# Kernel tuning notes

Measured on AMD Instinct MI355X. Metric: run time of the kernel, lower is better.

Reference implementation:

```python
import jax, jax.numpy as jnp
import numpy as np

# ---- constants from the source module ----
NB = [[0,1,2,3],[0,1,4],[0,2,5],[0,3,6],[1,4,7],[2,5,8],[3,6,9],[4,7,10],[5,8,11],[6,9],[7,10],[8,11],[12,13,14,15],[12,13,16],[12,14,17],[12,15],[13,16,18],[14,17,19],[16,18,20],[17,19,21],[18,20,22],[19,21,23],[20,22],[21,23]]
PARENT = np.array([0,0,0,0,1,2,3,4,5,6,7,8,9,9,9,12,13,14,16,17,18,19,20,21])  # root parent sentinel handled separately
KJ, NV, PREG = 24, 6890, 200
LEN = np.array([len(n) for n in NB])
NBR_IDX = np.zeros((KJ,4), np.int32)
NBR_VALID = np.zeros((KJ,4), np.float32)
for k, n in enumerate(NB):
    NBR_IDX[k,:len(n)] = n; NBR_VALID[k,:len(n)] = 1.0
BETA_POS = np.zeros((KJ,17), np.float32); BETA_POS[np.arange(KJ), 4*LEN] = 1.0
SLICE_MASK = np.zeros((23,17), np.float32)
for j in range(23):
    SLICE_MASK[j,:4*LEN[j]+1] = 1.0  # self.K[j] has 4*len(NB[j])+1 rows
NBR_IDX = jnp.asarray(NBR_IDX); NBR_VALID = jnp.asarray(NBR_VALID)
BETA_POS = jnp.asarray(BETA_POS); SLICE_MASK = jnpp = jnp.asarray(SLICE_MASK)


def setup_inputs() -> dict:
    key = jax.random.key(0)
    ks = jax.random.split(key, 9)
    V = jax.random.normal(ks[0], (PREG, NV, 3), jnp.float32)
    T = jax.random.normal(ks[1], (PREG, NV, 3), jnp.float32)
    J = jax.random.normal(ks[2], (PREG, KJ, 3), jnp.float32)
    theta = 0.3 * jax.random.normal(ks[3], (PREG, 72), jnp.float32)
    W_prime = jax.random.uniform(ks[4], (NV, KJ), jnp.float32)
    W_i = jax.random.uniform(ks[5], (NV, KJ), jnp.float32)
    W_i = W_i / W_i.sum(axis=1, keepdims=True)
    A = jax.random.uniform(ks[6], (23, NV), jnp.float32)
    K_mats = 0.01 * jax.random.normal(ks[7], (23, 17, 3 * NV), jnp.float32)
    K_mats = K_mats * SLICE_MASK[:, :, None]  # zero rows beyond the ragged per-joint size
    beta_2 = jnp.ones((1,), jnp.float32)
    return {"V": V, "T": T, "J": J, "theta": theta, "W_prime": W_prime, "W_i": W_i, "A": A, "K_mats": K_mats, "beta_2": beta_2, "epoch": 1}


def _rodrigues(pose):  # pose: (K,3)
    angle = jnp.maximum(jnp.linalg.norm(pose, axis=1, keepdims=True), 1e-8)
    axis = pose / angle
    x, y, z = axis[:, 0], axis[:, 1], axis[:, 2]
    zero = jnp.zeros_like(x)
    skew = jnp.stack([zero, -z, y, z, zero, -x, -y, x, zero], axis=1).reshape(-1, 3, 3)
    outer = axis[:, :, None] * axis[:, None, :]
    c = jnp.cos(angle)[:, :, None]
    s = jnp.sin(angle)[:, :, None]
    eye = jnp.eye(3, dtype=pose.dtype)[None]
    return c * eye + (1.0 - c) * outer + s * skew


def _compute_G(pose72, Jp):  # pose72: (72,), Jp: (K,3) -> (K,4,4)
    R = _rodrigues(pose72.reshape(KJ, 3))
    t = Jp - jnp.concatenate([jnp.zeros((1, 3), Jp.dtype), Jp[PARENT[1:]]], axis=0)
    G_local = jnp.zeros((KJ, 4, 4), Jp.dtype)
    G_local = G_local.at[:, :3, :3].set(R).at[:, :3, 3].set(t).at[:, 3, 3].set(1.0)
    Gs = [G_local[0]]
    for i in range(1, KJ):  # fixed 24-joint kinematic tree
        Gs.append(Gs[PARENT[i]] @ G_local[i])
    G = jnp.stack(Gs, axis=0)
    off = jnp.einsum('kij,kj->ki', G[:, :3, :3], Jp)  # homogeneous w=0 -> rotation only
    return G.at[:, :3, 3].add(-off)


def _axis2quat(p):  # (M,3) -> (M,4)
    angle = jnp.sqrt(jnp.maximum(jnp.sum(p ** 2, axis=1), 1e-16))
    n = p / angle[:, None]
    s = jnp.sin(angle / 2)
    return jnp.stack([n[:, 0] * s, n[:, 1] * s, n[:, 2] * s, jnp.cos(angle / 2) - 1.0], axis=1)


def reference(V, T, J, theta, W_prime, W_i, A, K_mats, beta_2, epoch):
    P = V.shape[0]
    b2 = beta_2[0]
    # normalized skinning weights
    W_relu = jax.nn.relu(W_prime)
    W_change = W_relu / (W_relu.sum(axis=1, keepdims=True) + 1e-8)
    # per-pose global joint transforms
    G_prime = jax.vmap(_compute_G)(theta, J)  # (P,K,4,4)
    # quaternion features and blend-shape correction
    q = _axis2quat(theta.reshape(P * KJ, 3)).reshape(P, KJ, 4)
    qg = q[:, NBR_IDX, :] * NBR_VALID[None, :, :, None]       # (P,K,4,4) neighbor gather
    q17 = jnp.concatenate([qg.reshape(P, KJ, 16), jnp.zeros((P, KJ, 1), q.dtype)], axis=-1)
    q17 = q17 + BETA_POS[None] * b2                            # beta_2 at column 4*len
    qm = q17[:, 1:, :] * SLICE_MASK[None]                      # ragged slice q_ne[:, j+1, :lenK]
    contrib = jnp.einsum('pjl,jlm->pjm', qm, K_mats).reshape(P, 23, NV, 3)
    T_p = jnp.einsum('pjnc,jn->pnc', contrib, jax.nn.relu(A)) + T
    # linear blend skinning
    T_h = jnp.concatenate([T_p, jnp.ones((P, NV, 1), T_p.dtype)], axis=-1)
    transformed = jnp.einsum('pkij,pnj->pnki', G_prime[:, :, :3, :], T_h)  # (P,N,K,3)
    verts = jnp.einsum('nk,pnkc->pnc', W_change, transformed)
    # energies
    e = float(epoch)
    g_wi = 0.1 * np.exp(-0.1 * e)
    g_w = 0.002 * np.exp(-0.008 * e)
    g_a = 0.001 * np.exp(-0.008 * e)
    g_k = 0.1 * np.exp(-0.008 * e)
    E_D = jnp.sum((V - verts) ** 2)
    E_Wi = jnp.sum((W_change - W_i) ** 2)
    E_W = jnp.sum(jnp.abs(W_change))
    E_A = jnp.sum(jnp.abs(A))
    E_K = jnp.sum(jnp.sqrt(jnp.sum(K_mats ** 2, axis=(1, 2))))
    E = E_D + g_wi * E_Wi + g_w * E_W + g_a * E_A + g_k * E_K
    return (E, verts)
```

## Files before the change

kernel.cpp:

```cpp
#include <hip/hip_runtime.h>
#include <math.h>

#define KJ 24
#define NV 6890
#define PREG 200
#define M_TOT (NV*3)
#define KDIM 391
#define KPAD 416
#define TP_STRIDE 20672
#define NMT64 323
#define NSTAGE (NMT64*13)

#define EDP_OFF 0
#define EKP_OFF 5400
#define WIP_OFF 101984
#define EWP_OFF 102016
#define EAP_OFF 102048
#define RED_OFF 102080
#define G_OFF   102112
#define TP_OFF  159712
#define QBH_OFF_U 10903488
#define QBL_OFF_U 11009984
#define BTH_OFF_U 11116480
#define BTL_OFF_U 19716032
#define TP2_OFF 14157792

typedef __attribute__((ext_vector_type(8))) short short8;
typedef __attribute__((ext_vector_type(4))) float f32x4;
typedef __attribute__((ext_vector_type(4))) unsigned int u32x4;

__constant__ int c_PARENT[24] = {0,0,0,0,1,2,3,4,5,6,7,8,9,9,9,12,13,14,16,17,18,19,20,21};
__constant__ int c_DEPTH[24]  = {0,1,1,1,2,2,2,3,3,3,4,4,4,4,4,5,5,5,6,6,7,7,8,8};
__constant__ int c_LEN[24]    = {4,3,3,3,3,3,3,3,3,2,2,2,4,3,3,2,3,3,3,3,3,3,2,2};
__constant__ int c_NBR[24][4] = {
  {0,1,2,3},{0,1,4,0},{0,2,5,0},{0,3,6,0},{1,4,7,0},{2,5,8,0},{3,6,9,0},{4,7,10,0},
  {5,8,11,0},{6,9,0,0},{7,10,0,0},{8,11,0,0},{12,13,14,15},{12,13,16,0},{12,14,17,0},
  {12,15,0,0},{13,16,18,0},{14,17,19,0},{16,18,20,0},{17,19,21,0},{18,20,22,0},
  {19,21,23,0},{20,22,0,0},{21,23,0,0}};

__device__ __forceinline__ float waveReduce(float v) {
  #pragma unroll
  for (int off = 32; off > 0; off >>= 1) v += __shfl_down(v, off, 64);
  return v;
}
__device__ __forceinline__ unsigned short f2bf(float x) {
  union { float f; unsigned u; } v; v.f = x;
  unsigned r = v.u + 0x7FFFu + ((v.u >> 16) & 1u);
  return (unsigned short)(r >> 16);
}
__device__ __forceinline__ float bf2f(unsigned short h) {
  union { unsigned u; float f; } v; v.u = ((unsigned)h) << 16; return v.f;
}

__global__ __launch_bounds__(256) void kPre(const float* __restrict__ J,
                                            const float* __restrict__ theta,
                                            const float* __restrict__ beta2,
                                            const float* __restrict__ Wp,
                                            const float* __restrict__ Wi,
                                            const float* __restrict__ A,
                                            const float* __restrict__ K,
                                            float* __restrict__ ws) {
  unsigned short* qbh = (unsigned short*)ws + QBH_OFF_U;
  unsigned short* qbl = (unsigned short*)ws + QBL_OFF_U;
  int b = blockIdx.x;
  if (b < 50) {
    __shared__ float Gl[4][24][12];
    __shared__ float Gg[4][24][12];
    __shared__ float q[4][24][4];
    int w = threadIdx.x >> 6, t = threadIdx.x & 63;
    int p = b*4 + w;
    if (t < 24) {
      float x = theta[p*72 + 3*t + 0];
      float y = theta[p*72 + 3*t + 1];
      float z = theta[p*72 + 3*t + 2];
      float n2 = x*x + y*y + z*z;
      float ang = fmaxf(sqrtf(n2), 1e-8f);
      float ia = 1.f/ang;
      float ax = x*ia, ay = y*ia, az = z*ia;
      float c = cosf(ang), s = sinf(ang), C = 1.f - c;
      float jx = J[p*72+3*t], jy = J[p*72+3*t+1], jz = J[p*72+3*t+2];
      float tx = jx, ty = jy, tz = jz;
      if (t > 0) {
        int par = c_PARENT[t];
        tx -= J[p*72+3*par]; ty -= J[p*72+3*par+1]; tz -= J[p*72+3*par+2];
      }
      Gl[w][t][0]=c+C*ax*ax;   Gl[w][t][1]=C*ax*ay-s*az; Gl[w][t][2]=C*ax*az+s*ay; Gl[w][t][3]=tx;
      Gl[w][t][4]=C*ax*ay+s*az;Gl[w][t][5]=c+C*ay*ay;    Gl[w][t][6]=C*ay*az-s*ax; Gl[w][t][7]=ty;
      Gl[w][t][8]=C*ax*az-s*ay;Gl[w][t][9]=C*ay*az+s*ax; Gl[w][t][10]=c+C*az*az;   Gl[w][t][11]=tz;
      float ang2 = sqrtf(fmaxf(n2, 1e-16f));
      float inv2 = 1.f/ang2;
      float s2 = sinf(0.5f*ang2);
      q[w][t][0] = x*inv2*s2; q[w][t][1] = y*inv2*s2; q[w][t][2] = z*inv2*s2;
      q[w][t][3] = cosf(0.5f*ang2) - 1.f;
    }
    __syncthreads();
    for (int lev = 0; lev <= 8; lev++) {
      if (t < 24 && c_DEPTH[t] == lev) {
        if (lev == 0) {
          for (int i2 = 0; i2 < 12; i2++) Gg[w][0][i2] = Gl[w][0][i2];
        } else {
          int par = c_PARENT[t];
          for (int r = 0; r < 3; r++) {
            float g0 = Gg[w][par][r*4+0], g1 = Gg[w][par][r*4+1];
            float g2 = Gg[w][par][r*4+2], g3 = Gg[w][par][r*4+3];
            for (int c2 = 0; c2 < 4; c2++) {
              float v = g0*Gl[w][t][0+c2] + g1*Gl[w][t][4+c2] + g2*Gl[w][t][8+c2];
              if (c2 == 3) v += g3;
              Gg[w][t][r*4+c2] = v;
            }
          }
        }
      }
      __syncthreads();
    }
    if (t < 24) {
      float jx = J[p*72+3*t], jy = J[p*72+3*t+1], jz = J[p*72+3*t+2];
      float* gp = ws + G_OFF + p*288 + t*12;
      #pragma unroll
      for (int r = 0; r < 3; r++) {
        float off = Gg[w][t][r*4+0]*jx + Gg[w][t][r*4+1]*jy + Gg[w][t][r*4+2]*jz;
        Gg[w][t][r*4+3] -= off;
      }
      #pragma unroll
      for (int i2 = 0; i2 < 12; i2++) gp[i2] = Gg[w][t][i2];
    }
    __syncthreads();
    float b2 = beta2[0];
    for (int e = t; e < KDIM; e += 64) {
      int j = e / 17, l = e - 17*j;
      int k = j + 1;
      float val = 0.f;
      if (l < 4*c_LEN[j] + 1) {
        if (l < 16) {
          int sidx = l >> 2, cc = l & 3;
          if (sidx < c_LEN[k]) val = q[w][c_NBR[k][sidx]][cc];
        }
        if (l == 4*c_LEN[k]) val += b2;
      }
      unsigned short hi = f2bf(val);
      unsigned short lo = f2bf(val - bf2f(hi));
      qbh[p*KPAD + e] = hi;
      qbl[p*KPAD + e] = lo;
    }
    for (int e = KDIM + t; e < KPAD; e += 64) {
      qbh[p*KPAD + e] = 0; qbl[p*KPAD + e] = 0;
    }
  } else if (b < 77) {
    int d = b - 50;
    int t = threadIdx.x;
    int n = d*256 + t;
    float ewi = 0.f, ew = 0.f, ea = 0.f;
    if (n < NV) {
      float wv[24]; float sum = 0.f;
      const float4* wp4 = (const float4*)(Wp + n*24);
      #pragma unroll
      for (int i = 0; i < 6; i++) {
        float4 v4 = wp4[i];
        wv[4*i+0] = fmaxf(v4.x, 0.f); wv[4*i+1] = fmaxf(v4.y, 0.f);
        wv[4*i+2] = fmaxf(v4.z, 0.f); wv[4*i+3] = fmaxf(v4.w, 0.f);
        sum += wv[4*i+0]+wv[4*i+1]+wv[4*i+2]+wv[4*i+3];
      }
      float inv = 1.f/(sum + 1e-8f);
      #pragma unroll
      for (int k = 0; k < 24; k++) {
        float wc = wv[k]*inv;
        ew += fabsf(wc);
        float dd = wc - Wi[n*24+k];
        ewi += dd*dd;
      }
    }
    for (int i = d*256 + t; i < 23*NV; i += 27*256) ea += fabsf(A[i]);
    for (int i = d*256 + t; i < 56*KPAD; i += 27*256) {
      qbh[200*KPAD + i] = 0; qbl[200*KPAD + i] = 0;
    }
    __shared__ float red[3][4];
    int lane = t & 63, wv2 = t >> 6;
    ewi = waveReduce(ewi); ew = waveReduce(ew); ea = waveReduce(ea);
    if (lane == 0) { red[0][wv2] = ewi; red[1][wv2] = ew; red[2][wv2] = ea; }
    __syncthreads();
    if (t == 0) {
      ws[WIP_OFF + d] = red[0][0]+red[0][1]+red[0][2]+red[0][3];
      ws[EWP_OFF + d] = red[1][0]+red[1][1]+red[1][2]+red[1][3];
      ws[EAP_OFF + d] = red[2][0]+red[2][1]+red[2][2]+red[2][3];
    }
  } else {
    int flat = b - 77;
    int bx = flat % NMT64, by = flat / NMT64;
    int m0 = bx*64, kg0 = by*32;
    __shared__ unsigned short Sh[32*66];
    __shared__ unsigned short Sl[32*66];
    __shared__ float ek[23];
    int t = threadIdx.x;
    if (t < 23) ek[t] = 0.f;
    __syncthreads();
    int krow = t >> 3, mseg = (t & 7) * 8;
    int kg = kg0 + krow;
    int mm = m0 + mseg;
    float kv[8], wv[8]; float sq = 0.f;
    #pragma unroll
    for (int i = 0; i < 8; i++) { kv[i] = 0.f; wv[i] = 0.f; }
    if (kg < KDIM) {
      const float* kr = K + (size_t)kg*M_TOT + mm;
      if (mm + 7 < M_TOT) {
        float4 a4 = *(const float4*)kr; float4 b4 = *(const float4*)(kr+4);
        kv[0]=a4.x; kv[1]=a4.y; kv[2]=a4.z; kv[3]=a4.w;
        kv[4]=b4.x; kv[5]=b4.y; kv[6]=b4.z; kv[7]=b4.w;
      } else {
        #pragma unroll
        for (int i = 0; i < 8; i++) if (mm+i < M_TOT) kv[i] = kr[i];
      }
      int j = kg / 17;
      int nb = mm / 3;
      float av[4];
      #pragma unroll
      for (int i = 0; i < 4; i++)
        av[i] = (nb + i < NV) ? fmaxf(A[j*NV + nb + i], 0.f) : 0.f;
      #pragma unroll
      for (int i = 0; i < 8; i++) {
        float a = (mm+i < M_TOT) ? av[(mm+i)/3 - nb] : 0.f;
        wv[i] = kv[i]*a;
        sq = fmaf(kv[i], kv[i], sq);
      }
    }
    #pragma unroll
    for (int c = 0; c < 4; c++) {
      unsigned short h0 = f2bf(wv[2*c]),  h1 = f2bf(wv[2*c+1]);
      unsigned short l0 = f2bf(wv[2*c]   - bf2f(h0));
      unsigned short l1 = f2bf(wv[2*c+1] - bf2f(h1));
      *(unsigned*)&Sh[krow*66 + mseg + 2*c] = (unsigned)h0 | ((unsigned)h1 << 16);
      *(unsigned*)&Sl[krow*66 + mseg + 2*c] = (unsigned)l0 | ((unsigned)l1 << 16);
    }
    sq += __shfl_xor(sq, 1, 64);
    sq += __shfl_xor(sq, 2, 64);
    sq += __shfl_xor(sq, 4, 64);
    if ((t & 7) == 0 && kg < KDIM) atomicAdd(&ek[kg/17], sq);
    __syncthreads();
    int mrow = t >> 2, kq = t & 3;
    unsigned dh[4], dl[4];
    #pragma unroll
    for (int c2 = 0; c2 < 4; c2++) {
      unsigned short s0 = Sh[(kq*8 + 2*c2    )*66 + mrow];
      unsigned short s1 = Sh[(kq*8 + 2*c2 + 1)*66 + mrow];
      dh[c2] = (unsigned)s0 | ((unsigned)s1 << 16);
      unsigned short u0 = Sl[(kq*8 + 2*c2    )*66 + mrow];
      unsigned short u1 = Sl[(kq*8 + 2*c2 + 1)*66 + mrow];
      dl[c2] = (unsigned)u0 | ((unsigned)u1 << 16);
    }
    unsigned short* BtH = (unsigned short*)ws + BTH_OFF_U;
    unsigned short* BtL = (unsigned short*)ws + BTL_OFF_U;
    size_t o = (size_t)(m0 + mrow)*KPAD + kg0 + kq*8;
    *(u32x4*)(BtH + o) = (u32x4){dh[0], dh[1], dh[2], dh[3]};
    *(u32x4*)(BtL + o) = (u32x4){dl[0], dl[1], dl[2], dl[3]};
    if (t < 23) ws[EKP_OFF + t*NSTAGE + flat] = ek[t];
  }
}

template<int KS0, int NKS>
__device__ __forceinline__ void kb_body(const unsigned short* __restrict__ qbh,
                                        const unsigned short* __restrict__ qbl,
                                        const unsigned short* __restrict__ BtH,
                                        const unsigned short* __restrict__ BtL,
                                        short (*__restrict__ SBh)[64*32],
                                        short (*__restrict__ SBl)[64*32],
                                        float* __restrict__ TPd, int m0) {
  const int tid = threadIdx.x;
  const int w = tid >> 6, lane = tid & 63;
  const int r = lane & 15, qd = lane >> 4;

  f32x4 acc[4][4];
  #pragma unroll
  for (int h = 0; h < 4; h++)
    #pragma unroll
    for (int f = 0; f < 4; f++) acc[h][f] = (f32x4){0.f,0.f,0.f,0.f};

  int aofs[4];
  #pragma unroll
  for (int h = 0; h < 4; h++) aofs[h] = (w*64 + h*16 + r)*KPAD + KS0*32 + qd*8;

  const int srow = tid >> 2, sseg = tid & 3;
  const size_t gB = (size_t)(m0 + srow)*KPAD + KS0*32 + sseg*8;
  const int swr = ((srow >> 4)*64 + sseg*16 + (srow & 15)) * 8;

  short8 ah[2][4], al[2][4];
  short8 bsh[2], bsl[2];

  bsh[0] = *(const short8*)(BtH + gB);
  bsl[0] = *(const short8*)(BtL + gB);
  #pragma unroll
  for (int h = 0; h < 4; h++) {
    ah[0][h] = *(const short8*)(qbh + aofs[h]);
    al[0][h] = *(const short8*)(qbl + aofs[h]);
  }
  *(short8*)&SBh[0][swr] = bsh[0];
  *(short8*)&SBl[0][swr] = bsl[0];
  bsh[1] = *(const short8*)(BtH + gB + 32);
  bsl[1] = *(const short8*)(BtL + gB + 32);
  #pragma unroll
  for (int h = 0; h < 4; h++) {
    ah[1][h] = *(const short8*)(qbh + aofs[h] + 32);
    al[1][h] = *(const short8*)(qbl + aofs[h] + 32);
  }
  __syncthreads();

  #pragma unroll
  for (int ks = 0; ks < NKS; ks++) {
    const int cur = ks & 1, nxt = cur ^ 1;
    short8 bfh[4], bfl[4];
    #pragma unroll
    for (int f = 0; f < 4; f++) {
      bfh[f] = *(const short8*)&SBh[cur][(f*64 + lane)*8];
      bfl[f] = *(const short8*)&SBl[cur][(f*64 + lane)*8];
    }
    #pragma unroll
    for (int f = 0; f < 4; f++)
      #pragma unroll
      for (int h = 0; h < 4; h++) {
        acc[h][f] = __builtin_amdgcn_mfma_f32_16x16x32_bf16(ah[cur][h], bfh[f], acc[h][f], 0, 0, 0);
        acc[h][f] = __builtin_amdgcn_mfma_f32_16x16x32_bf16(ah[cur][h], bfl[f], acc[h][f], 0, 0, 0);
        acc[h][f] = __builtin_amdgcn_mfma_f32_16x16x32_bf16(al[cur][h], bfh[f], acc[h][f], 0, 0, 0);
      }
    if (ks + 1 < NKS) {
      *(short8*)&SBh[nxt][swr] = bsh[nxt];
      *(short8*)&SBl[nxt][swr] = bsl[nxt];
    }
    if (ks + 2 < NKS) {
      const int o = (ks + 2) * 32;
      bsh[cur] = *(const short8*)(BtH + gB + o);
      bsl[cur] = *(const short8*)(BtL + gB + o);
      #pragma unroll
      for (int h = 0; h < 4; h++) {
        ah[cur][h] = *(const short8*)(qbh + aofs[h] + o);
        al[cur][h] = *(const short8*)(qbl + aofs[h] + o);
      }
    }
    __syncthreads();
  }
  #pragma unroll
  for (int h = 0; h < 4; h++)
    #pragma unroll
    for (int f = 0; f < 4; f++)
      #pragma unroll
      for (int g = 0; g < 4; g++) {
        int p = w*64 + h*16 + qd*4 + g;
        if (p < PREG)
          TPd[(size_t)p*TP_STRIDE + m0 + f*16 + r] = acc[h][f][g];
      }
}

__global__ __launch_bounds__(256) void kB(float* __restrict__ ws) {
  __shared__ short SBh[2][64*32];
  __shared__ short SBl[2][64*32];
  const unsigned short* qbh = (const unsigned short*)ws + QBH_OFF_U;
  const unsigned short* qbl = (const unsigned short*)ws + QBL_OFF_U;
  const unsigned short* BtH = (const unsigned short*)ws + BTH_OFF_U;
  const unsigned short* BtL = (const unsigned short*)ws + BTL_OFF_U;
  const int m0 = blockIdx.x * 64;
  if (blockIdx.y == 0)
    kb_body<0, 7>(qbh, qbl, BtH, BtL, SBh, SBl, ws + TP_OFF, m0);
  else
    kb_body<7, 6>(qbh, qbl, BtH, BtL, SBh, SBl, ws + TP2_OFF, m0);
}

__global__ __launch_bounds__(256) void kC(const float* __restrict__ V,
                                          const float* __restrict__ T,
                                          const float* __restrict__ Wp,
                                          const float* __restrict__ ws,
                                          float* __restrict__ out) {
  int p0 = blockIdx.y * 8;
  int n = blockIdx.x*256 + threadIdx.x;
  __shared__ float tmp[4];
  float ed = 0.f;
  if (n < NV) {
    float wv[24]; float sum = 0.f;
    const float4* wp4 = (const float4*)(Wp + n*24);
    #pragma unroll
    for (int i = 0; i < 6; i++) {
      float4 v4 = wp4[i];
      wv[4*i+0] = fmaxf(v4.x, 0.f); wv[4*i+1] = fmaxf(v4.y, 0.f);
      wv[4*i+2] = fmaxf(v4.z, 0.f); wv[4*i+3] = fmaxf(v4.w, 0.f);
      sum += wv[4*i+0]+wv[4*i+1]+wv[4*i+2]+wv[4*i+3];
    }
    float inv = 1.f/(sum + 1e-8f);
    for (int pp = 0; pp < 8; pp++) {
      int p = p0 + pp;
      const float* __restrict__ gp = ws + G_OFF + (size_t)p*288;
      float M[12];
      #pragma unroll
      for (int i = 0; i < 12; i++) M[i] = 0.f;
      #pragma unroll
      for (int k = 0; k < 24; k++) {
        float wc = wv[k];
        #pragma unroll
        for (int i = 0; i < 12; i++)
          M[i] = fmaf(wc, gp[k*12 + i], M[i]);
      }
      #pragma unroll
      for (int i = 0; i < 12; i++) M[i] *= inv;
      size_t tb = (size_t)p*M_TOT + 3*n;
      size_t pb = (size_t)p*TP_STRIDE + 3*n;
      float t0 = ws[TP_OFF + pb + 0] + ws[TP2_OFF + pb + 0] + T[tb + 0];
      float t1 = ws[TP_OFF + pb + 1] + ws[TP2_OFF + pb + 1] + T[tb + 1];
      float t2 = ws[TP_OFF + pb + 2] + ws[TP2_OFF + pb + 2] + T[tb + 2];
      float v0 = M[0]*t0 + M[1]*t1 + M[2]*t2  + M[3];
      float v1 = M[4]*t0 + M[5]*t1 + M[6]*t2  + M[7];
      float v2 = M[8]*t0 + M[9]*t1 + M[10]*t2 + M[11];
      out[1+tb+0] = v0; out[1+tb+1] = v1; out[1+tb+2] = v2;
      float d0 = V[tb+0]-v0, d1 = V[tb+1]-v1, d2 = V[tb+2]-v2;
      ed += d0*d0 + d1*d1 + d2*d2;
    }
  }
  ed = waveReduce(ed);
  int lane = threadIdx.x & 63, w = threadIdx.x >> 6;
  if (lane == 0) tmp[w] = ed;
  __syncthreads();
  if (threadIdx.x == 0)
    ((float*)ws)[EDP_OFF + blockIdx.y*27 + blockIdx.x] = tmp[0]+tmp[1]+tmp[2]+tmp[3];
}

__global__ __launch_bounds__(256) void kF1(float* __restrict__ ws) {
  __shared__ float sb[4];
  int b = blockIdx.x, t = threadIdx.x, lane = t & 63, w = t >> 6;
  if (b < 23) {
    float s = 0.f;
    for (int i = t; i < NSTAGE; i += 256) s += ws[EKP_OFF + b*NSTAGE + i];
    s = waveReduce(s);
    if (lane == 0) sb[w] = s;
    __syncthreads();
    if (t == 0) ws[RED_OFF + b] = sb[0]+sb[1]+sb[2]+sb[3];
  } else if (b == 23) {
    float s = 0.f;
    for (int i = t; i < 675; i += 256) s += ws[EDP_OFF + i];
    s = waveReduce(s);
    if (lane == 0) sb[w] = s;
    __syncthreads();
    if (t == 0) ws[RED_OFF + 23] = sb[0]+sb[1]+sb[2]+sb[3];
  } else {
    if (w == 0) {
      float s = (lane < 27) ? ws[WIP_OFF + lane] : 0.f;
      s = waveReduce(s);
      if (lane == 0) ws[RED_OFF + 24] = s;
    } else if (w == 1) {
      float s = (lane < 27) ? ws[EWP_OFF + lane] : 0.f;
      s = waveReduce(s);
      if (lane == 0) ws[RED_OFF + 25] = s;
    } else if (w == 2) {
      float s = (lane < 27) ? ws[EAP_OFF + lane] : 0.f;
      s = waveReduce(s);
      if (lane == 0) ws[RED_OFF + 26] = s;
    }
  }
}

__global__ void kF2(const int* __restrict__ epoch, const float* __restrict__ ws,
                    float* __restrict__ out) {
  int t = threadIdx.x;
  float s = (t < 23) ? sqrtf(ws[RED_OFF + t]) : 0.f;
  s = waveReduce(s);
  if (t == 0) {
    float e    = (float)epoch[0];
    float g_wi = 0.1f   * expf(-0.1f  * e);
    float g_w  = 0.002f * expf(-0.008f* e);
    float g_a  = 0.001f * expf(-0.008f* e);
    float g_k  = 0.1f   * expf(-0.008f* e);
    out[0] = ws[RED_OFF+23] + g_wi*ws[RED_OFF+24] + g_w*ws[RED_OFF+25]
           + g_a*ws[RED_OFF+26] + g_k*s;
  }
}

extern "C" void kernel_launch(void* const* d_in, const int* in_sizes, int n_in,
                              void* d_out, int out_size, void* d_ws, size_t ws_size,
                              hipStream_t stream) {
  const float* V     = (const float*)d_in[0];
  const float* T     = (const float*)d_in[1];
  const float* J     = (const float*)d_in[2];
  const float* theta = (const float*)d_in[3];
  const float* Wp    = (const float*)d_in[4];
  const float* Wi    = (const float*)d_in[5];
  const float* A     = (const float*)d_in[6];
  const float* K     = (const float*)d_in[7];
  const float* b2    = (const float*)d_in[8];
  const int*   epoch = (const int*)d_in[9];
  float* out = (float*)d_out;
  float* ws  = (float*)d_ws;

  hipLaunchKernelGGL(kPre, dim3(77 + NSTAGE), dim3(256), 0, stream,
                     J, theta, b2, Wp, Wi, A, K, ws);
  hipLaunchKernelGGL(kB,   dim3(NMT64, 2),    dim3(256), 0, stream, ws);
  hipLaunchKernelGGL(kC,   dim3(27, 25),      dim3(256), 0, stream, V, T, Wp, ws, out);
  hipLaunchKernelGGL(kF1,  dim3(25),          dim3(256), 0, stream, ws);
  hipLaunchKernelGGL(kF2,  dim3(1),           dim3(64),  0, stream, epoch, ws, out);
}
```

Baseline: 179.4 us.

## Fuse K-matrix bf16 split/transpose staging into the GEMM kernel

Before, a separate pass inside kPre read K, scaled it by relu(A), split it into hi/lo bf16 halves, and wrote transposed copies to workspace, which kB then read back. Now kB loads K directly from global memory, scales it using an A tile cached in shared memory, transposes and converts it in LDS, and feeds the MFMA loop with the K loads for the next step issued early. This removes the write and re-read of the large BtH/BtL buffers and cuts the kPre grid to 77 blocks. In exchange the GEMM loop does more ALU work and adds an extra barrier per k-step, and the per-joint norm partials are now gathered per kB block.

```diff
diff --git a/kernel.cpp b/kernel.cpp
--- a/kernel.cpp
+++ b/kernel.cpp
@@ -9,7 +9,7 @@
 #define KPAD 416
 #define TP_STRIDE 20672
 #define NMT64 323
-#define NSTAGE (NMT64*13)
+#define NKB (NMT64*2)
 
 #define EDP_OFF 0
 #define EKP_OFF 5400
@@ -21,8 +21,6 @@
 #define TP_OFF  159712
 #define QBH_OFF_U 10903488
 #define QBL_OFF_U 11009984
-#define BTH_OFF_U 11116480
-#define BTL_OFF_U 19716032
 #define TP2_OFF 14157792
 
 typedef __attribute__((ext_vector_type(8))) short short8;
@@ -58,7 +56,6 @@
                                             const float* __restrict__ Wp,
                                             const float* __restrict__ Wi,
                                             const float* __restrict__ A,
-                                            const float* __restrict__ K,
                                             float* __restrict__ ws) {
   unsigned short* qbh = (unsigned short*)ws + QBH_OFF_U;
   unsigned short* qbl = (unsigned short*)ws + QBL_OFF_U;
@@ -145,7 +142,7 @@
     for (int e = KDIM + t; e < KPAD; e += 64) {
       qbh[p*KPAD + e] = 0; qbl[p*KPAD + e] = 0;
     }
-  } else if (b < 77) {
+  } else {
     int d = b - 50;
     int t = threadIdx.x;
     int n = d*256 + t;
@@ -183,22 +180,55 @@
       ws[EWP_OFF + d] = red[1][0]+red[1][1]+red[1][2]+red[1][3];
       ws[EAP_OFF + d] = red[2][0]+red[2][1]+red[2][2]+red[2][3];
     }
-  } else {
-    int flat = b - 77;
-    int bx = flat % NMT64, by = flat / NMT64;
-    int m0 = bx*64, kg0 = by*32;
-    __shared__ unsigned short Sh[32*66];
-    __shared__ unsigned short Sl[32*66];
-    __shared__ float ek[23];
-    int t = threadIdx.x;
-    if (t < 23) ek[t] = 0.f;
-    __syncthreads();
-    int krow = t >> 3, mseg = (t & 7) * 8;
-    int kg = kg0 + krow;
-    int mm = m0 + mseg;
-    float kv[8], wv[8]; float sq = 0.f;
-    #pragma unroll
-    for (int i = 0; i < 8; i++) { kv[i] = 0.f; wv[i] = 0.f; }
+  }
+}
+
+template<int KS0, int NKS, int JMIN>
+__device__ __forceinline__ void kb_body(const float* __restrict__ A,
+                                        const float* __restrict__ K,
+                                        const unsigned short* __restrict__ qbh,
+                                        const unsigned short* __restrict__ qbl,
+                                        float* __restrict__ Sk,
+                                        short (*__restrict__ SBh)[64*32],
+                                        short (*__restrict__ SBl)[64*32],
+                                        float (*__restrict__ SA)[24],
+                                        float* __restrict__ ek,
+                                        float* __restrict__ ws,
+                                        float* __restrict__ TPd,
+                                        int m0, int flat) {
+  const int tid = threadIdx.x;
+  const int w = tid >> 6, lane = tid & 63;
+  const int r = lane & 15, qd = lane >> 4;
+  const int krow = tid >> 3, mseg = (tid & 7) * 8;
+  const int mm = m0 + mseg;
+  const int nb0 = m0 / 3;
+  const int mrow2 = tid >> 2, kq2 = tid & 3;
+  const int swr = ((mrow2 >> 4)*64 + kq2*16 + (mrow2 & 15)) * 8;
+
+  if (tid < 23) ek[tid] = 0.f;
+  for (int i = tid; i < 14*24; i += 256) {
+    int jj = i / 24, nn = i - jj*24;
+    int j2 = JMIN + jj, n2 = nb0 + nn;
+    ((float*)SA)[i] = (j2 < 23 && n2 < NV) ? fmaxf(A[j2*NV + n2], 0.f) : 0.f;
+  }
+
+  f32x4 acc[4][4];
+  #pragma unroll
+  for (int h = 0; h < 4; h++)
+    #pragma unroll
+    for (int f = 0; f < 4; f++) acc[h][f] = (f32x4){0.f,0.f,0.f,0.f};
+
+  int aofs[4];
+  #pragma unroll
+  for (int h = 0; h < 4; h++) aofs[h] = (w*64 + h*16 + r)*KPAD + KS0*32 + qd*8;
+
+  short8 ah[2][4], al[2][4];
+  float kv[8];
+
+  auto loadK = [&](int ks) {
+    int kg = (KS0 + ks)*32 + krow;
+    #pragma unroll
+    for (int i = 0; i < 8; i++) kv[i] = 0.f;
     if (kg < KDIM) {
       const float* kr = K + (size_t)kg*M_TOT + mm;
       if (mm + 7 < M_TOT) {
@@ -209,12 +239,19 @@
         #pragma unroll
         for (int i = 0; i < 8; i++) if (mm+i < M_TOT) kv[i] = kr[i];
       }
-      int j = kg / 17;
+    }
+  };
+  auto stageK = [&](int ks) {
+    int kg = (KS0 + ks)*32 + krow;
+    float wv[8]; float sq = 0.f;
+    #pragma unroll
+    for (int i = 0; i < 8; i++) wv[i] = 0.f;
+    if (kg < KDIM) {
+      int jj = kg/17 - JMIN;
       int nb = mm / 3;
       float av[4];
       #pragma unroll
-      for (int i = 0; i < 4; i++)
-        av[i] = (nb + i < NV) ? fmaxf(A[j*NV + nb + i], 0.f) : 0.f;
+      for (int i = 0; i < 4; i++) av[i] = SA[jj][nb - nb0 + i];
       #pragma unroll
       for (int i = 0; i < 8; i++) {
         float a = (mm+i < M_TOT) ? av[(mm+i)/3 - nb] : 0.f;
@@ -223,78 +260,39 @@
       }
     }
     #pragma unroll
-    for (int c = 0; c < 4; c++) {
-      unsigned short h0 = f2bf(wv[2*c]),  h1 = f2bf(wv[2*c+1]);
-      unsigned short l0 = f2bf(wv[2*c]   - bf2f(h0));
-      unsigned short l1 = f2bf(wv[2*c+1] - bf2f(h1));
-      *(unsigned*)&Sh[krow*66 + mseg + 2*c] = (unsigned)h0 | ((unsigned)h1 << 16);
-      *(unsigned*)&Sl[krow*66 + mseg + 2*c] = (unsigned)l0 | ((unsigned)l1 << 16);
-    }
+    for (int c = 0; c < 4; c++)
+      *(float2*)&Sk[krow*66 + mseg + 2*c] = make_float2(wv[2*c], wv[2*c+1]);
     sq += __shfl_xor(sq, 1, 64);
     sq += __shfl_xor(sq, 2, 64);
     sq += __shfl_xor(sq, 4, 64);
-    if ((t & 7) == 0 && kg < KDIM) atomicAdd(&ek[kg/17], sq);
-    __syncthreads();
-    int mrow = t >> 2, kq = t & 3;
+    if ((tid & 7) == 0 && kg < KDIM) atomicAdd(&ek[kg/17], sq);
+  };
+  auto xpose = [&](int buf) {
+    float vv[8];
+    #pragma unroll
+    for (int j = 0; j < 8; j++) vv[j] = Sk[(kq2*8 + j)*66 + mrow2];
     unsigned dh[4], dl[4];
     #pragma unroll
-    for (int c2 = 0; c2 < 4; c2++) {
-      unsigned short s0 = Sh[(kq*8 + 2*c2    )*66 + mrow];
-      unsigned short s1 = Sh[(kq*8 + 2*c2 + 1)*66 + mrow];
-      dh[c2] = (unsigned)s0 | ((unsigned)s1 << 16);
-      unsigned short u0 = Sl[(kq*8 + 2*c2    )*66 + mrow];
-      unsigned short u1 = Sl[(kq*8 + 2*c2 + 1)*66 + mrow];
-      dl[c2] = (unsigned)u0 | ((unsigned)u1 << 16);
-    }
-    unsigned short* BtH = (unsigned short*)ws + BTH_OFF_U;
-    unsigned short* BtL = (unsigned short*)ws + BTL_OFF_U;
-    size_t o = (size_t)(m0 + mrow)*KPAD + kg0 + kq*8;
-    *(u32x4*)(BtH + o) = (u32x4){dh[0], dh[1], dh[2], dh[3]};
-    *(u32x4*)(BtL + o) = (u32x4){dl[0], dl[1], dl[2], dl[3]};
-    if (t < 23) ws[EKP_OFF + t*NSTAGE + flat] = ek[t];
-  }
-}
-
-template<int KS0, int NKS>
-__device__ __forceinline__ void kb_body(const unsigned short* __restrict__ qbh,
-                                        const unsigned short* __restrict__ qbl,
-                                        const unsigned short* __restrict__ BtH,
-                                        const unsigned short* __restrict__ BtL,
-                                        short (*__restrict__ SBh)[64*32],
-                                        short (*__restrict__ SBl)[64*32],
-                                        float* __restrict__ TPd, int m0) {
-  const int tid = threadIdx.x;
-  const int w = tid >> 6, lane = tid & 63;
-  const int r = lane & 15, qd = lane >> 4;
-
-  f32x4 acc[4][4];
-  #pragma unroll
-  for (int h = 0; h < 4; h++)
-    #pragma unroll
-    for (int f = 0; f < 4; f++) acc[h][f] = (f32x4){0.f,0.f,0.f,0.f};
-
-  int aofs[4];
-  #pragma unroll
-  for (int h = 0; h < 4; h++) aofs[h] = (w*64 + h*16 + r)*KPAD + KS0*32 + qd*8;
-
-  const int srow = tid >> 2, sseg = tid & 3;
-  const size_t gB = (size_t)(m0 + srow)*KPAD + KS0*32 + sseg*8;
-  const int swr = ((srow >> 4)*64 + sseg*16 + (srow & 15)) * 8;
-
-  short8 ah[2][4], al[2][4];
-  short8 bsh[2], bsl[2];
-
-  bsh[0] = *(const short8*)(BtH + gB);
-  bsl[0] = *(const short8*)(BtL + gB);
+    for (int c = 0; c < 4; c++) {
+      unsigned short h0 = f2bf(vv[2*c]),   h1 = f2bf(vv[2*c+1]);
+      unsigned short l0 = f2bf(vv[2*c]   - bf2f(h0));
+      unsigned short l1 = f2bf(vv[2*c+1] - bf2f(h1));
+      dh[c] = (unsigned)h0 | ((unsigned)h1 << 16);
+      dl[c] = (unsigned)l0 | ((unsigned)l1 << 16);
+    }
+    *(u32x4*)&SBh[buf][swr] = (u32x4){dh[0], dh[1], dh[2], dh[3]};
+    *(u32x4*)&SBl[buf][swr] = (u32x4){dl[0], dl[1], dl[2], dl[3]};
+  };
+
+  loadK(0);
   #pragma unroll
   for (int h = 0; h < 4; h++) {
     ah[0][h] = *(const short8*)(qbh + aofs[h]);
     al[0][h] = *(const short8*)(qbl + aofs[h]);
   }
-  *(short8*)&SBh[0][swr] = bsh[0];
-  *(short8*)&SBl[0][swr] = bsl[0];
-  bsh[1] = *(const short8*)(BtH + gB + 32);
-  bsl[1] = *(const short8*)(BtL + gB + 32);
+  stageK(0);
+  __syncthreads();
+  xpose(0);
   #pragma unroll
   for (int h = 0; h < 4; h++) {
     ah[1][h] = *(const short8*)(qbh + aofs[h] + 32);
@@ -305,6 +303,7 @@
   #pragma unroll
   for (int ks = 0; ks < NKS; ks++) {
     const int cur = ks & 1, nxt = cur ^ 1;
+    if (ks + 1 < NKS) loadK(ks + 1);
     short8 bfh[4], bfl[4];
     #pragma unroll
     for (int f = 0; f < 4; f++) {
@@ -319,14 +318,9 @@
         acc[h][f] = __builtin_amdgcn_mfma_f32_16x16x32_bf16(ah[cur][h], bfl[f], acc[h][f], 0, 0, 0);
         acc[h][f] = __builtin_amdgcn_mfma_f32_16x16x32_bf16(al[cur][h], bfh[f], acc[h][f], 0, 0, 0);
       }
-    if (ks + 1 < NKS) {
-      *(short8*)&SBh[nxt][swr] = bsh[nxt];
-      *(short8*)&SBl[nxt][swr] = bsl[nxt];
-    }
+    if (ks + 1 < NKS) stageK(ks + 1);
     if (ks + 2 < NKS) {
       const int o = (ks + 2) * 32;
-      bsh[cur] = *(const short8*)(BtH + gB + o);
-      bsl[cur] = *(const short8*)(BtL + gB + o);
       #pragma unroll
       for (int h = 0; h < 4; h++) {
         ah[cur][h] = *(const short8*)(qbh + aofs[h] + o);
@@ -334,7 +328,11 @@
       }
     }
     __syncthreads();
-  }
+    if (ks + 1 < NKS) xpose(nxt);
+    __syncthreads();
+  }
+
+  if (tid < 23) ws[EKP_OFF + tid*NKB + flat] = ek[tid];
   #pragma unroll
   for (int h = 0; h < 4; h++)
     #pragma unroll
@@ -347,18 +345,22 @@
       }
 }
 
-__global__ __launch_bounds__(256) void kB(float* __restrict__ ws) {
+__global__ __launch_bounds__(256) void kB(const float* __restrict__ A,
+                                          const float* __restrict__ K,
+                                          float* __restrict__ ws) {
+  __shared__ float Sk[32*66];
   __shared__ short SBh[2][64*32];
   __shared__ short SBl[2][64*32];
+  __shared__ float SA[14][24];
+  __shared__ float ek[23];
   const unsigned short* qbh = (const unsigned short*)ws + QBH_OFF_U;
   const unsigned short* qbl = (const unsigned short*)ws + QBL_OFF_U;
-  const unsigned short* BtH = (const unsigned short*)ws + BTH_OFF_U;
-  const unsigned short* BtL = (const unsigned short*)ws + BTL_OFF_U;
   const int m0 = blockIdx.x * 64;
+  const int flat = blockIdx.x + blockIdx.y * NMT64;
   if (blockIdx.y == 0)
-    kb_body<0, 7>(qbh, qbl, BtH, BtL, SBh, SBl, ws + TP_OFF, m0);
+    kb_body<0, 7, 0>(A, K, qbh, qbl, Sk, SBh, SBl, SA, ek, ws, ws + TP_OFF,  m0, flat);
   else
-    kb_body<7, 6>(qbh, qbl, BtH, BtL, SBh, SBl, ws + TP2_OFF, m0);
+    kb_body<7, 6, 13>(A, K, qbh, qbl, Sk, SBh, SBl, SA, ek, ws, ws + TP2_OFF, m0, flat);
 }
 
 __global__ __launch_bounds__(256) void kC(const float* __restrict__ V,
@@ -422,7 +424,7 @@
   int b = blockIdx.x, t = threadIdx.x, lane = t & 63, w = t >> 6;
   if (b < 23) {
     float s = 0.f;
-    for (int i = t; i < NSTAGE; i += 256) s += ws[EKP_OFF + b*NSTAGE + i];
+    for (int i = t; i < NKB; i += 256) s += ws[EKP_OFF + b*NKB + i];
     s = waveReduce(s);
     if (lane == 0) sb[w] = s;
     __syncthreads();
@@ -483,10 +485,10 @@
   float* out = (float*)d_out;
   float* ws  = (float*)d_ws;
 
-  hipLaunchKernelGGL(kPre, dim3(77 + NSTAGE), dim3(256), 0, stream,
-                     J, theta, b2, Wp, Wi, A, K, ws);
-  hipLaunchKernelGGL(kB,   dim3(NMT64, 2),    dim3(256), 0, stream, ws);
-  hipLaunchKernelGGL(kC,   dim3(27, 25),      dim3(256), 0, stream, V, T, Wp, ws, out);
-  hipLaunchKernelGGL(kF1,  dim3(25),          dim3(256), 0, stream, ws);
-  hipLaunchKernelGGL(kF2,  dim3(1),           dim3(64),  0, stream, epoch, ws, out);
-}
+  hipLaunchKernelGGL(kPre, dim3(77),        dim3(256), 0, stream,
+                     J, theta, b2, Wp, Wi, A, ws);
+  hipLaunchKernelGGL(kB,   dim3(NMT64, 2),  dim3(256), 0, stream, A, K, ws);
+  hipLaunchKernelGGL(kC,   dim3(27, 25),    dim3(256), 0, stream, V, T, Wp, ws, out);
+  hipLaunchKernelGGL(kF1,  dim3(25),        dim3(256), 0, stream, ws);
+  hipLaunchKernelGGL(kF2,  dim3(1),         dim3(64),  0, stream, epoch, ws, out);
+}
```

Result: faster. 175.6 us (median of 2 runs) (-2.2%).
